# Optimization experiments

Measured on AMD Instinct MI355X. Metric: run time of the kernel, lower is better.

Reference implementation:

```python
import jax, jax.numpy as jnp
import numpy as np

N_NODES = 100000
N_EDGES = 1600000
IN_DIM = 128
HIDDEN = 128


def setup_inputs() -> dict:
    key = jax.random.key(0)
    ks = jax.random.split(key, 8)
    x = jax.random.normal(ks[0], (N_NODES, IN_DIM), dtype=jnp.float32)
    edge_index = jax.random.randint(ks[1], (2, N_EDGES), 0, N_NODES, dtype=jnp.int32)
    # GCNConv weights (glorot-style scale) and biases
    s1 = 1.0 / np.sqrt(IN_DIM)
    s2 = 1.0 / np.sqrt(HIDDEN)
    W1 = jax.random.normal(ks[2], (IN_DIM, HIDDEN), dtype=jnp.float32) * s1
    b1 = jnp.zeros((HIDDEN,), dtype=jnp.float32)
    W2 = jax.random.normal(ks[3], (HIDDEN, HIDDEN), dtype=jnp.float32) * s2
    b2 = jnp.zeros((HIDDEN,), dtype=jnp.float32)
    Wout = jax.random.normal(ks[4], (HIDDEN, 1), dtype=jnp.float32) * s2
    bout = jnp.zeros((1,), dtype=jnp.float32)
    return {"x": x, "edge_index": edge_index, "W1": W1, "b1": b1,
            "W2": W2, "b2": b2, "Wout": Wout, "bout": bout}


def _gcn_conv(x, row, col, norm, W, b, n_nodes):
    # x' = D^-1/2 (A + I) D^-1/2 (x W) + b   (PyG GCNConv, symmetric norm)
    xw = x @ W                                   # [N, H] dense GEMM
    msg = xw[row] * norm[:, None]                # gather + scale  [E+N, H]
    out = jax.ops.segment_sum(msg, col, num_segments=n_nodes)  # scatter-add
    return out + b


def reference(x, edge_index, W1, b1, W2, b2, Wout, bout):
    n = x.shape[0]
    self_idx = jnp.arange(n, dtype=edge_index.dtype)
    row = jnp.concatenate([edge_index[0], self_idx])   # sources (+ self loops)
    col = jnp.concatenate([edge_index[1], self_idx])   # targets (+ self loops)
    deg = jax.ops.segment_sum(jnp.ones_like(col, x.dtype), col, num_segments=n)
    dis = jax.lax.rsqrt(deg)                            # deg >= 1 (self loops)
    norm = dis[row] * dis[col]                          # [E+N]
    h = jax.nn.relu(_gcn_conv(x, row, col, norm, W1, b1, n))
    h = jax.nn.relu(_gcn_conv(h, row, col, norm, W2, b2, n))
    # mlp_layers=1 -> empty Sequential; dropout identity at inference
    return (h @ Wout + bout).squeeze(-1)                # [N]
```

## Files before the change

### kernel.cpp

```cpp
#include <hip/hip_runtime.h>


typedef __attribute__((ext_vector_type(8))) short bf16x8;
typedef __attribute__((ext_vector_type(4))) float f32x4;
typedef _Float16 f16x4 __attribute__((ext_vector_type(4)));
typedef _Float16 f16x8 __attribute__((ext_vector_type(8)));

__device__ __forceinline__ unsigned short bf16_rn(float f) {
  unsigned u = __builtin_bit_cast(unsigned, f);
  u += 0x7FFFu + ((u >> 16) & 1u);
  return (unsigned short)(u >> 16);
}

__global__ __launch_bounds__(256) void fill_k(const int* __restrict__ row,
                                              const int* __restrict__ col,
                                              int* __restrict__ cnt,
                                              int* __restrict__ bkt,
                                              int E, int N) {
  int g = blockIdx.x & 7;
  int bg = blockIdx.x >> 3;
  int bpg = gridDim.x >> 3;
  int nd8 = N >> 3;
  int lo = g * nd8, hi = lo + nd8;
  int chunk = (E + bpg - 1) / bpg;
  int e0 = bg * chunk;
  int e1 = e0 + chunk; if (e1 > E) e1 = E;
  for (int e = e0 + threadIdx.x; e < e1; e += 256) {
    int c = __builtin_nontemporal_load(col + e);
    if (c >= lo && c < hi) {
      int r = __builtin_nontemporal_load(row + e);
      int pos = atomicAdd(&cnt[c], 1);
      if (pos < 64) bkt[(size_t)c * 64 + pos] = r;
    }
  }
}

__global__ void dis_k(const int* __restrict__ cnt, float* __restrict__ dis, int n) {
  int i = blockIdx.x * blockDim.x + threadIdx.x;
  if (i < n) dis[i] = rsqrtf((float)(cnt[i] + 1));
}

__global__ void wprep_k(const float* __restrict__ W, short* __restrict__ wh,
                        short* __restrict__ wl) {
  int t = blockIdx.x * 256 + threadIdx.x;
  int j = t & 7, l = (t >> 3) & 63, ct = (t >> 9) & 7, ks = t >> 12;
  int k = ks * 32 + ((l >> 4) * 8) + j;
  int c = ct * 16 + (l & 15);
  float w = W[k * 128 + c];
  unsigned short h = bf16_rn(w);
  float hf = __builtin_bit_cast(float, (unsigned)h << 16);
  wh[t] = (short)h;
  wl[t] = (short)bf16_rn(w - hf);
}

__device__ __forceinline__ void bf16_split(float v, short& hi, short& lo) {
  __bf16 h = (__bf16)v;
  hi = __builtin_bit_cast(short, h);
  float hf = (float)h;
  lo = __builtin_bit_cast(short, (__bf16)(v - hf));
}

__global__ __launch_bounds__(256) void gemm_mfma_k(const float* __restrict__ A,
                                                   const short* __restrict__ whp,
                                                   const short* __restrict__ wlp,
                                                   const float* __restrict__ dis,
                                                   _Float16* __restrict__ Y, int n) {
  __shared__ _Float16 lds[4][32][136];
  int lane = threadIdx.x & 63;
  int wave = threadIdx.x >> 6;
  long row0 = ((long)blockIdx.x * 4 + wave) * 32;
  if (row0 >= n) return;
  int mr = lane & 15, kg = lane >> 4;
  const float* arow0 = A + (row0 + mr) * 128 + kg * 8;
  const float* arow1 = A + (row0 + 16 + mr) * 128 + kg * 8;
  const bf16x8* WH = (const bf16x8*)whp;
  const bf16x8* WL = (const bf16x8*)wlp;
  f32x4 acc0[8], acc1[8];
#pragma unroll
  for (int ct = 0; ct < 8; ++ct) {
    acc0[ct] = (f32x4){0.f, 0.f, 0.f, 0.f};
    acc1[ct] = (f32x4){0.f, 0.f, 0.f, 0.f};
  }
#pragma unroll
  for (int ks = 0; ks < 4; ++ks) {
    f32x4 a00 = *(const f32x4*)(arow0 + ks * 32);
    f32x4 a01 = *(const f32x4*)(arow0 + ks * 32 + 4);
    f32x4 a10 = *(const f32x4*)(arow1 + ks * 32);
    f32x4 a11 = *(const f32x4*)(arow1 + ks * 32 + 4);
    bf16x8 ah0, al0, ah1, al1;
#pragma unroll
    for (int j = 0; j < 4; ++j) {
      short h, l;
      bf16_split(a00[j], h, l); ah0[j] = h;     al0[j] = l;
      bf16_split(a01[j], h, l); ah0[4 + j] = h; al0[4 + j] = l;
      bf16_split(a10[j], h, l); ah1[j] = h;     al1[j] = l;
      bf16_split(a11[j], h, l); ah1[4 + j] = h; al1[4 + j] = l;
    }
#pragma unroll
    for (int ct = 0; ct < 8; ++ct) {
      bf16x8 bh = WH[(ks * 8 + ct) * 64 + lane];
      bf16x8 bl = WL[(ks * 8 + ct) * 64 + lane];
      acc0[ct] = __builtin_amdgcn_mfma_f32_16x16x32_bf16(ah0, bh, acc0[ct], 0, 0, 0);
      acc1[ct] = __builtin_amdgcn_mfma_f32_16x16x32_bf16(ah1, bh, acc1[ct], 0, 0, 0);
      acc0[ct] = __builtin_amdgcn_mfma_f32_16x16x32_bf16(al0, bh, acc0[ct], 0, 0, 0);
      acc1[ct] = __builtin_amdgcn_mfma_f32_16x16x32_bf16(al1, bh, acc1[ct], 0, 0, 0);
      acc0[ct] = __builtin_amdgcn_mfma_f32_16x16x32_bf16(ah0, bl, acc0[ct], 0, 0, 0);
      acc1[ct] = __builtin_amdgcn_mfma_f32_16x16x32_bf16(ah1, bl, acc1[ct], 0, 0, 0);
    }
  }
  float sc0[4], sc1[4];
#pragma unroll
  for (int j = 0; j < 4; ++j) {
    sc0[j] = dis[row0 + kg * 4 + j];
    sc1[j] = dis[row0 + 16 + kg * 4 + j];
  }
  _Float16* tile = &lds[wave][0][0];
#pragma unroll
  for (int ct = 0; ct < 8; ++ct)
#pragma unroll
    for (int j = 0; j < 4; ++j) {
      tile[(kg * 4 + j) * 136 + ct * 16 + mr]        = (_Float16)(acc0[ct][j] * sc0[j]);
      tile[(16 + kg * 4 + j) * 136 + ct * 16 + mr]   = (_Float16)(acc1[ct][j] * sc1[j]);
    }
  __builtin_amdgcn_s_waitcnt(0);
#pragma unroll
  for (int i = 0; i < 8; ++i) {
    int chunk = lane + 64 * i;
    int r = chunk >> 4, c8 = chunk & 15;
    *(f16x8*)(Y + (row0 + r) * 128 + c8 * 8) = *(const f16x8*)(tile + r * 136 + c8 * 8);
  }
}

__device__ __forceinline__ float4 agg_core(const f16x4* __restrict__ Y,
                                           const int* __restrict__ cnt,
                                           const int* __restrict__ bkt,
                                           int c, int r) {
  int m = cnt[c]; if (m > 64) m = 64;
  int idxA = 0;
  if (r < m) idxA = __builtin_nontemporal_load(&bkt[(size_t)c * 64 + r]);
  f16x4 sv = Y[(size_t)c * 32 + r];
  float4 acc = make_float4((float)sv[0], (float)sv[1], (float)sv[2], (float)sv[3]);
  int mA = m < 32 ? m : 32;
  int j = 0;
  for (; j + 8 <= mA; j += 8) {
    f16x4 v[8];
#pragma unroll
    for (int q = 0; q < 8; ++q) {
      int s = __shfl(idxA, j + q, 32);
      v[q] = Y[(size_t)s * 32 + r];
    }
#pragma unroll
    for (int q = 0; q < 8; ++q) {
      acc.x += (float)v[q][0]; acc.y += (float)v[q][1];
      acc.z += (float)v[q][2]; acc.w += (float)v[q][3];
    }
  }
  for (; j < mA; ++j) {
    int s = __shfl(idxA, j, 32);
    f16x4 v = Y[(size_t)s * 32 + r];
    acc.x += (float)v[0]; acc.y += (float)v[1];
    acc.z += (float)v[2]; acc.w += (float)v[3];
  }
  if (m > 32) {
    int idxB = 0;
    if (32 + r < m) idxB = __builtin_nontemporal_load(&bkt[(size_t)c * 64 + 32 + r]);
    for (j = 32; j < m; ++j) {
      int s = __shfl(idxB, j - 32, 32);
      f16x4 v = Y[(size_t)s * 32 + r];
      acc.x += (float)v[0]; acc.y += (float)v[1];
      acc.z += (float)v[2]; acc.w += (float)v[3];
    }
  }
  return acc;
}

__global__ __launch_bounds__(256) void agg_mid_k(const _Float16* __restrict__ y,
                                                 const float* __restrict__ dis,
                                                 const int* __restrict__ cnt,
                                                 const int* __restrict__ bkt,
                                                 const float* __restrict__ bias,
                                                 float* __restrict__ h, int n) {
  int c = (blockIdx.x * 256 + threadIdx.x) >> 5;
  if (c >= n) return;
  int r = threadIdx.x & 31;
  float4 acc = agg_core((const f16x4*)y, cnt, bkt, c, r);
  float d = dis[c];
  float4 b = *(const float4*)&bias[r * 4];
  float4 o;
  o.x = fmaxf(fmaf(acc.x, d, b.x), 0.f);
  o.y = fmaxf(fmaf(acc.y, d, b.y), 0.f);
  o.z = fmaxf(fmaf(acc.z, d, b.z), 0.f);
  o.w = fmaxf(fmaf(acc.w, d, b.w), 0.f);
  *(float4*)&h[(size_t)c * 128 + r * 4] = o;
}

__global__ __launch_bounds__(256) void agg_final_k(const _Float16* __restrict__ y,
                                                   const float* __restrict__ dis,
                                                   const int* __restrict__ cnt,
                                                   const int* __restrict__ bkt,
                                                   const float* __restrict__ bias,
                                                   const float* __restrict__ Wout,
                                                   const float* __restrict__ bout,
                                                   float* __restrict__ out, int n) {
  int c = (blockIdx.x * 256 + threadIdx.x) >> 5;
  if (c >= n) return;
  int r = threadIdx.x & 31;
  float4 acc = agg_core((const f16x4*)y, cnt, bkt, c, r);
  float d = dis[c];
  float4 b = *(const float4*)&bias[r * 4];
  float4 w4 = *(const float4*)&Wout[r * 4];
  float hx = fmaxf(fmaf(acc.x, d, b.x), 0.f);
  float hy = fmaxf(fmaf(acc.y, d, b.y), 0.f);
  float hz = fmaxf(fmaf(acc.z, d, b.z), 0.f);
  float hw = fmaxf(fmaf(acc.w, d, b.w), 0.f);
  float partial = hx * w4.x + hy * w4.y + hz * w4.z + hw * w4.w;
#pragma unroll
  for (int off = 16; off > 0; off >>= 1) partial += __shfl_down(partial, off, 32);
  if (r == 0) out[c] = partial + bout[0];
}

extern "C" void kernel_launch(void* const* d_in, const int* in_sizes, int n_in,
                              void* d_out, int out_size, void* d_ws, size_t ws_size,
                              hipStream_t stream) {
  const float* x    = (const float*)d_in[0];
  const int*   ei   = (const int*)d_in[1];
  const float* W1   = (const float*)d_in[2];
  const float* b1   = (const float*)d_in[3];
  const float* W2   = (const float*)d_in[4];
  const float* b2   = (const float*)d_in[5];
  const float* Wout = (const float*)d_in[6];
  const float* bout = (const float*)d_in[7];
  float* out = (float*)d_out;

  const int N = in_sizes[0] / 128;
  const int E = in_sizes[1] / 2;
  const int* row = ei;
  const int* col = ei + E;

  char* ws = (char*)d_ws;
  size_t cur = 0;
  auto alloc = [&](size_t bytes) -> void* {
    cur = (cur + 255) & ~(size_t)255;
    void* p = ws + cur;
    cur += bytes;
    return p;
  };
  _Float16* y   = (_Float16*)alloc((size_t)N * 128 * 2);
  float*    h   = (float*)alloc((size_t)N * 128 * 4);
  int*      bkt = (int*)alloc((size_t)N * 64 * 4);
  int*      cnt = (int*)alloc((size_t)N * 4);
  float*    dis = (float*)alloc((size_t)N * 4);
  short*    wh1 = (short*)alloc(16384 * 2);
  short*    wl1 = (short*)alloc(16384 * 2);
  short*    wh2 = (short*)alloc(16384 * 2);
  short*    wl2 = (short*)alloc(16384 * 2);
  (void)ws_size; (void)n_in; (void)out_size;

  const int gN = (N + 255) / 256;
  const int gGemm = (N + 127) / 128;
  const int gAgg = (N + 7) / 8;

  wprep_k<<<64, 256, 0, stream>>>(W1, wh1, wl1);
  wprep_k<<<64, 256, 0, stream>>>(W2, wh2, wl2);

  (void)hipMemsetAsync(cnt, 0, (size_t)N * 4, stream);
  fill_k<<<2048, 256, 0, stream>>>(row, col, cnt, bkt, E, N);
  dis_k<<<gN, 256, 0, stream>>>(cnt, dis, N);

  gemm_mfma_k<<<gGemm, 256, 0, stream>>>(x, wh1, wl1, dis, y, N);
  agg_mid_k<<<gAgg, 256, 0, stream>>>(y, dis, cnt, bkt, b1, h, N);

  gemm_mfma_k<<<gGemm, 256, 0, stream>>>(h, wh2, wl2, dis, y, N);
  agg_final_k<<<gAgg, 256, 0, stream>>>(y, dis, cnt, bkt, b2, Wout, bout, out, N);
}
```

Baseline: 342.8 us.

## Stage split weights in LDS for GEMM and vectorize edge bucketing loads

Measured after the change: 338.6 us. No clear change (-1.2%).

```diff
diff --git a/kernel.cpp b/kernel.cpp
--- a/kernel.cpp
+++ b/kernel.cpp
@@ -3,6 +3,7 @@
 
 typedef __attribute__((ext_vector_type(8))) short bf16x8;
 typedef __attribute__((ext_vector_type(4))) float f32x4;
+typedef __attribute__((ext_vector_type(4))) int i32x4;
 typedef _Float16 f16x4 __attribute__((ext_vector_type(4)));
 typedef _Float16 f16x8 __attribute__((ext_vector_type(8)));
 
@@ -22,15 +23,24 @@
   int bpg = gridDim.x >> 3;
   int nd8 = N >> 3;
   int lo = g * nd8, hi = lo + nd8;
-  int chunk = (E + bpg - 1) / bpg;
+  int E4 = E >> 2;
+  int chunk = (E4 + bpg - 1) / bpg;
   int e0 = bg * chunk;
-  int e1 = e0 + chunk; if (e1 > E) e1 = E;
+  int e1 = e0 + chunk; if (e1 > E4) e1 = E4;
+  const i32x4* col4 = (const i32x4*)col;
+  const i32x4* row4 = (const i32x4*)row;
   for (int e = e0 + threadIdx.x; e < e1; e += 256) {
-    int c = __builtin_nontemporal_load(col + e);
-    if (c >= lo && c < hi) {
-      int r = __builtin_nontemporal_load(row + e);
-      int pos = atomicAdd(&cnt[c], 1);
-      if (pos < 64) bkt[(size_t)c * 64 + pos] = r;
+    i32x4 c4 = __builtin_nontemporal_load(col4 + e);
+    bool p0 = (c4[0] >= lo) & (c4[0] < hi);
+    bool p1 = (c4[1] >= lo) & (c4[1] < hi);
+    bool p2 = (c4[2] >= lo) & (c4[2] < hi);
+    bool p3 = (c4[3] >= lo) & (c4[3] < hi);
+    if (p0 | p1 | p2 | p3) {
+      i32x4 r4 = __builtin_nontemporal_load(row4 + e);
+      if (p0) { int p = atomicAdd(&cnt[c4[0]], 1); if (p < 64) bkt[(size_t)c4[0] * 64 + p] = r4[0]; }
+      if (p1) { int p = atomicAdd(&cnt[c4[1]], 1); if (p < 64) bkt[(size_t)c4[1] * 64 + p] = r4[1]; }
+      if (p2) { int p = atomicAdd(&cnt[c4[2]], 1); if (p < 64) bkt[(size_t)c4[2] * 64 + p] = r4[2]; }
+      if (p3) { int p = atomicAdd(&cnt[c4[3]], 1); if (p < 64) bkt[(size_t)c4[3] * 64 + p] = r4[3]; }
     }
   }
 }
@@ -65,62 +75,81 @@
                                                    const short* __restrict__ wlp,
                                                    const float* __restrict__ dis,
                                                    _Float16* __restrict__ Y, int n) {
-  __shared__ _Float16 lds[4][32][136];
-  int lane = threadIdx.x & 63;
-  int wave = threadIdx.x >> 6;
+  __shared__ short wlds[32768];
+  int tid = threadIdx.x;
+  int lane = tid & 63, wave = tid >> 6;
   long row0 = ((long)blockIdx.x * 4 + wave) * 32;
-  if (row0 >= n) return;
+  bool active = row0 < n;
+
+  {
+    const bf16x8* sh = (const bf16x8*)whp;
+    const bf16x8* sl = (const bf16x8*)wlp;
+    bf16x8* dh = (bf16x8*)wlds;
+    bf16x8* dl = (bf16x8*)(wlds + 16384);
+#pragma unroll
+    for (int i = 0; i < 8; ++i) {
+      dh[tid + 256 * i] = sh[tid + 256 * i];
+      dl[tid + 256 * i] = sl[tid + 256 * i];
+    }
+  }
+  __syncthreads();
+
   int mr = lane & 15, kg = lane >> 4;
-  const float* arow0 = A + (row0 + mr) * 128 + kg * 8;
-  const float* arow1 = A + (row0 + 16 + mr) * 128 + kg * 8;
-  const bf16x8* WH = (const bf16x8*)whp;
-  const bf16x8* WL = (const bf16x8*)wlp;
   f32x4 acc0[8], acc1[8];
-#pragma unroll
-  for (int ct = 0; ct < 8; ++ct) {
-    acc0[ct] = (f32x4){0.f, 0.f, 0.f, 0.f};
-    acc1[ct] = (f32x4){0.f, 0.f, 0.f, 0.f};
-  }
-#pragma unroll
-  for (int ks = 0; ks < 4; ++ks) {
-    f32x4 a00 = *(const f32x4*)(arow0 + ks * 32);
-    f32x4 a01 = *(const f32x4*)(arow0 + ks * 32 + 4);
-    f32x4 a10 = *(const f32x4*)(arow1 + ks * 32);
-    f32x4 a11 = *(const f32x4*)(arow1 + ks * 32 + 4);
-    bf16x8 ah0, al0, ah1, al1;
-#pragma unroll
-    for (int j = 0; j < 4; ++j) {
-      short h, l;
-      bf16_split(a00[j], h, l); ah0[j] = h;     al0[j] = l;
-      bf16_split(a01[j], h, l); ah0[4 + j] = h; al0[4 + j] = l;
-      bf16_split(a10[j], h, l); ah1[j] = h;     al1[j] = l;
-      bf16_split(a11[j], h, l); ah1[4 + j] = h; al1[4 + j] = l;
-    }
+  if (active) {
+    const float* arow0 = A + (row0 + mr) * 128 + kg * 8;
+    const float* arow1 = A + (row0 + 16 + mr) * 128 + kg * 8;
+    const bf16x8* WH = (const bf16x8*)wlds;
+    const bf16x8* WL = (const bf16x8*)(wlds + 16384);
 #pragma unroll
     for (int ct = 0; ct < 8; ++ct) {
-      bf16x8 bh = WH[(ks * 8 + ct) * 64 + lane];
-      bf16x8 bl = WL[(ks * 8 + ct) * 64 + lane];
-      acc0[ct] = __builtin_amdgcn_mfma_f32_16x16x32_bf16(ah0, bh, acc0[ct], 0, 0, 0);
-      acc1[ct] = __builtin_amdgcn_mfma_f32_16x16x32_bf16(ah1, bh, acc1[ct], 0, 0, 0);
-      acc0[ct] = __builtin_amdgcn_mfma_f32_16x16x32_bf16(al0, bh, acc0[ct], 0, 0, 0);
-      acc1[ct] = __builtin_amdgcn_mfma_f32_16x16x32_bf16(al1, bh, acc1[ct], 0, 0, 0);
-      acc0[ct] = __builtin_amdgcn_mfma_f32_16x16x32_bf16(ah0, bl, acc0[ct], 0, 0, 0);
-      acc1[ct] = __builtin_amdgcn_mfma_f32_16x16x32_bf16(ah1, bl, acc1[ct], 0, 0, 0);
-    }
-  }
+      acc0[ct] = (f32x4){0.f, 0.f, 0.f, 0.f};
+      acc1[ct] = (f32x4){0.f, 0.f, 0.f, 0.f};
+    }
+#pragma unroll
+    for (int ks = 0; ks < 4; ++ks) {
+      f32x4 a00 = *(const f32x4*)(arow0 + ks * 32);
+      f32x4 a01 = *(const f32x4*)(arow0 + ks * 32 + 4);
+      f32x4 a10 = *(const f32x4*)(arow1 + ks * 32);
+      f32x4 a11 = *(const f32x4*)(arow1 + ks * 32 + 4);
+      bf16x8 ah0, al0, ah1, al1;
+#pragma unroll
+      for (int j = 0; j < 4; ++j) {
+        short h, l;
+        bf16_split(a00[j], h, l); ah0[j] = h;     al0[j] = l;
+        bf16_split(a01[j], h, l); ah0[4 + j] = h; al0[4 + j] = l;
+        bf16_split(a10[j], h, l); ah1[j] = h;     al1[j] = l;
+        bf16_split(a11[j], h, l); ah1[4 + j] = h; al1[4 + j] = l;
+      }
+#pragma unroll
+      for (int ct = 0; ct < 8; ++ct) {
+        bf16x8 bh = WH[(ks * 8 + ct) * 64 + lane];
+        bf16x8 bl = WL[(ks * 8 + ct) * 64 + lane];
+        acc0[ct] = __builtin_amdgcn_mfma_f32_16x16x32_bf16(ah0, bh, acc0[ct], 0, 0, 0);
+        acc1[ct] = __builtin_amdgcn_mfma_f32_16x16x32_bf16(ah1, bh, acc1[ct], 0, 0, 0);
+        acc0[ct] = __builtin_amdgcn_mfma_f32_16x16x32_bf16(al0, bh, acc0[ct], 0, 0, 0);
+        acc1[ct] = __builtin_amdgcn_mfma_f32_16x16x32_bf16(al1, bh, acc1[ct], 0, 0, 0);
+        acc0[ct] = __builtin_amdgcn_mfma_f32_16x16x32_bf16(ah0, bl, acc0[ct], 0, 0, 0);
+        acc1[ct] = __builtin_amdgcn_mfma_f32_16x16x32_bf16(ah1, bl, acc1[ct], 0, 0, 0);
+      }
+    }
+  }
+  __syncthreads();
+
+  if (!active) return;
   float sc0[4], sc1[4];
 #pragma unroll
   for (int j = 0; j < 4; ++j) {
     sc0[j] = dis[row0 + kg * 4 + j];
     sc1[j] = dis[row0 + 16 + kg * 4 + j];
   }
-  _Float16* tile = &lds[wave][0][0];
+  _Float16* tile = (_Float16*)wlds + wave * 4352;
 #pragma unroll
   for (int ct = 0; ct < 8; ++ct)
 #pragma unroll
     for (int j = 0; j < 4; ++j) {
-      tile[(kg * 4 + j) * 136 + ct * 16 + mr]        = (_Float16)(acc0[ct][j] * sc0[j]);
-      tile[(16 + kg * 4 + j) * 136 + ct * 16 + mr]   = (_Float16)(acc1[ct][j] * sc1[j]);
+      tile[(kg * 4 + j) * 136 + ct * 16 + mr]      = (_Float16)(acc0[ct][j] * sc0[j]);
+      tile[(16 + kg * 4 + j) * 136 + ct * 16 + mr] = (_Float16)(acc1[ct][j] * sc1[j]);
     }
   __builtin_amdgcn_s_waitcnt(0);
 #pragma unroll
```
